# Kernel tuning notes

Hardware: AMD Instinct MI355X
Metric: run time of the kernel (lower is better)

## Reference

```python
import jax, jax.numpy as jnp
import numpy as np

B, H, S, D = 16, 12, 1024, 64  # batch, heads, seq, head_dim (dim=768, num_head=12)


def setup_inputs() -> dict:
    key = jax.random.key(0)
    ks = jax.random.split(key, 9)
    sc = 1.0 / np.sqrt(D)
    return {
        "x": jax.random.normal(ks[0], (B, H, S, D), dtype=jnp.float32),
        "Wq": jax.random.normal(ks[1], (D, D), dtype=jnp.float32) * sc,
        "bq": jax.random.normal(ks[2], (D,), dtype=jnp.float32) * 0.02,
        "Wk": jax.random.normal(ks[3], (D, D), dtype=jnp.float32) * sc,
        "bk": jax.random.normal(ks[4], (D,), dtype=jnp.float32) * 0.02,
        "Wv": jax.random.normal(ks[5], (D, D), dtype=jnp.float32) * sc,
        "bv": jax.random.normal(ks[6], (D,), dtype=jnp.float32) * 0.02,
        "Wo": jax.random.normal(ks[7], (D, D), dtype=jnp.float32) * sc,
        "bo": jax.random.normal(ks[8], (D,), dtype=jnp.float32) * 0.02,
    }


def reference(x, Wq, bq, Wk, bk, Wv, bv, Wo, bo):
    # torch Linear: y = x @ W^T + b, applied to last dim (head_dim)
    q = jnp.einsum("bhsd,ed->bhse", x, Wq) + bq
    k = jnp.einsum("bhsd,ed->bhse", x, Wk) + bk
    v = jnp.einsum("bhsd,ed->bhse", x, Wv) + bv
    scores = jnp.einsum("bhqd,bhkd->bhqk", q, k) / jnp.sqrt(jnp.float32(q.shape[-1]))
    attn = jax.nn.softmax(scores, axis=-1)
    out = jnp.einsum("bhqk,bhkd->bhqd", attn, v)
    out = jnp.einsum("bhsd,ed->bhse", out, Wo) + bo
    return out
```

## Files before the change

kernel.cpp:

```cpp
#include <hip/hip_runtime.h>
#include <math.h>


typedef __bf16 bf16x8 __attribute__((ext_vector_type(8)));
typedef float  f32x4  __attribute__((ext_vector_type(4)));

#define MFMA(a, b, c) __builtin_amdgcn_mfma_f32_16x16x32_bf16((a), (b), (c), 0, 0, 0)

static constexpr int S = 1024;
static constexpr int PAD = 72;
static constexpr size_t NE = 196608ull * 64ull;
static constexpr float QSCALE = 0.125f * 1.4426950408889634f;

__device__ inline unsigned long long pack4bf(float a, float b, float c, float d) {
    union { __bf16 h[4]; unsigned long long u; } pk;
    pk.h[0] = (__bf16)a; pk.h[1] = (__bf16)b; pk.h[2] = (__bf16)c; pk.h[3] = (__bf16)d;
    return pk.u;
}

union frag_u { bf16x8 v; unsigned long long u[2]; };

__global__ __launch_bounds__(256, 3) void projkv(
    const float* __restrict__ x,
    const float* __restrict__ Wk, const float* __restrict__ bk,
    const float* __restrict__ Wv, const float* __restrict__ bv,
    __bf16* __restrict__ gk, __bf16* __restrict__ gvt)
{
    __shared__ __align__(16) __bf16 lx[128][PAD];
    __shared__ __align__(16) __bf16 lbuf[128][PAD];
    __shared__ __align__(16) __bf16 lw[2][8][64][8];
    __shared__ float lb[2][64];

    const int tid = threadIdx.x;
    const int row_base = blockIdx.x * 128;

    #pragma unroll
    for (int i = tid * 4; i < 8192; i += 1024) {
        float4 v = *(const float4*)(x + (size_t)row_base * 64 + i);
        int r = i >> 6, c = i & 63;
        *(unsigned long long*)&lx[r][c] = pack4bf(v.x, v.y, v.z, v.w);
    }
    #pragma unroll
    for (int c = tid; c < 1024; c += 256) {
        int mtx = c >> 9, rest = c & 511;
        int fe = rest >> 6, ln = rest & 63;
        int mm = ln & 15, qq = ln >> 4;
        int et = fe >> 1, half = fe & 1;
        const float* src = (mtx ? Wv : Wk) + (size_t)(et * 16 + mm) * 64 + half * 32 + qq * 8;
        float4 u0 = *(const float4*)(src);
        float4 u1 = *(const float4*)(src + 4);
        *(unsigned long long*)&lw[mtx][fe][ln][0] = pack4bf(u0.x, u0.y, u0.z, u0.w);
        *(unsigned long long*)&lw[mtx][fe][ln][4] = pack4bf(u1.x, u1.y, u1.z, u1.w);
    }
    if (tid < 64) { lb[0][tid] = bk[tid]; lb[1][tid] = bv[tid]; }
    __syncthreads();

    const int w = tid >> 6, lane = tid & 63, m = lane & 15, quad = lane >> 4;
    const int bh = row_base >> 10;
    const int s_base = row_base & 1023;

    bf16x8 xf[2][2];
    #pragma unroll
    for (int g = 0; g < 2; g++) {
        xf[g][0] = *(const bf16x8*)&lx[w * 32 + g * 16 + m][quad * 8];
        xf[g][1] = *(const bf16x8*)&lx[w * 32 + g * 16 + m][32 + quad * 8];
    }

    #pragma unroll
    for (int et = 0; et < 4; et++) {
        bf16x8 wf0 = *(const bf16x8*)&lw[0][et * 2 + 0][lane][0];
        bf16x8 wf1 = *(const bf16x8*)&lw[0][et * 2 + 1][lane][0];
        float4 bias = *(const float4*)&lb[0][et * 16 + quad * 4];
        #pragma unroll
        for (int g = 0; g < 2; g++) {
            f32x4 acc = {0.f, 0.f, 0.f, 0.f};
            acc = MFMA(wf0, xf[g][0], acc);
            acc = MFMA(wf1, xf[g][1], acc);
            *(unsigned long long*)&lbuf[w * 32 + g * 16 + m][et * 16 + quad * 4] =
                pack4bf(acc[0] + bias.x, acc[1] + bias.y,
                        acc[2] + bias.z, acc[3] + bias.w);
        }
    }
    __syncthreads();
    #pragma unroll
    for (int it = 0; it < 4; it++) {
        int idx = it * 256 + tid;
        int row = idx >> 3, col = (idx & 7) * 8;
        *(uint4*)(gk + ((size_t)row_base + row) * 64 + col) = *(uint4*)&lbuf[row][col];
    }
    __syncthreads();

    __bf16 (*lvt)[136] = (__bf16(*)[136])&lbuf[0][0];
    #pragma unroll
    for (int et = 0; et < 4; et++) {
        bf16x8 wf0 = *(const bf16x8*)&lw[1][et * 2 + 0][lane][0];
        bf16x8 wf1 = *(const bf16x8*)&lw[1][et * 2 + 1][lane][0];
        const float bias = lb[1][et * 16 + m];
        #pragma unroll
        for (int g = 0; g < 2; g++) {
            f32x4 acc = {0.f, 0.f, 0.f, 0.f};
            acc = MFMA(xf[g][0], wf0, acc);
            acc = MFMA(xf[g][1], wf1, acc);
            const int tp = (2 * w + g) & 3;
            const int p0 = 64 * (w >> 1) + 32 * (tp >> 1) + 8 * quad + 4 * (tp & 1);
            *(unsigned long long*)&lvt[et * 16 + m][p0] =
                pack4bf(acc[0] + bias, acc[1] + bias, acc[2] + bias, acc[3] + bias);
        }
    }
    __syncthreads();
    #pragma unroll
    for (int it = 0; it < 4; it++) {
        int idx = it * 256 + tid;
        int row = idx >> 4, col = (idx & 15) * 8;
        *(uint4*)(gvt + ((size_t)bh * 64 + row) * 1024 + s_base + col) = *(uint4*)&lvt[row][col];
    }
}

__global__ __launch_bounds__(512, 4) void attn(
    const float* __restrict__ x,
    const float* __restrict__ Wq, const float* __restrict__ bq,
    const __bf16* __restrict__ gk, const __bf16* __restrict__ gvt,
    const float* __restrict__ Wo, const float* __restrict__ bo,
    float* __restrict__ out)
{
    __shared__ __align__(16) union {
        __bf16 xq[256][PAD];
        struct {
            __bf16 k[64][PAD];
            __bf16 v[64][PAD];
        } m;
    } L;

    const int tid = threadIdx.x;
    const int w = tid >> 6, lane = tid & 63, m = lane & 15, quad = lane >> 4;
    const int bh = blockIdx.x;
    const int q0 = blockIdx.y * 256 + w * 32;

    const float* xq32 = x + ((size_t)bh * 1024 + blockIdx.y * 256) * 64;
    #pragma unroll
    for (int i = tid * 4; i < 16384; i += 2048) {
        float4 v = *(const float4*)(xq32 + i);
        int r = i >> 6, c = i & 63;
        *(unsigned long long*)&L.xq[r][c] = pack4bf(v.x, v.y, v.z, v.w);
    }
    __syncthreads();

    bf16x8 xqf[2][2];
    #pragma unroll
    for (int g = 0; g < 2; g++) {
        xqf[g][0] = *(const bf16x8*)&L.xq[w * 32 + g * 16 + m][quad * 8];
        xqf[g][1] = *(const bf16x8*)&L.xq[w * 32 + g * 16 + m][32 + quad * 8];
    }
    #pragma unroll
    for (int et = 0; et < 4; et++) {
        const float* wqrow = Wq + (size_t)(et * 16 + m) * 64;
        float4 a0 = *(const float4*)(wqrow + quad * 8);
        float4 a1 = *(const float4*)(wqrow + quad * 8 + 4);
        float4 a2 = *(const float4*)(wqrow + 32 + quad * 8);
        float4 a3 = *(const float4*)(wqrow + 36 + quad * 8);
        frag_u wf0, wf1;
        wf0.u[0] = pack4bf(a0.x, a0.y, a0.z, a0.w);
        wf0.u[1] = pack4bf(a1.x, a1.y, a1.z, a1.w);
        wf1.u[0] = pack4bf(a2.x, a2.y, a2.z, a2.w);
        wf1.u[1] = pack4bf(a3.x, a3.y, a3.z, a3.w);
        float4 bias = *(const float4*)(bq + et * 16 + quad * 4);
        #pragma unroll
        for (int g = 0; g < 2; g++) {
            f32x4 acc = {0.f, 0.f, 0.f, 0.f};
            acc = MFMA(wf0.v, xqf[g][0], acc);
            acc = MFMA(wf1.v, xqf[g][1], acc);
            *(unsigned long long*)&L.xq[w * 32 + g * 16 + m][et * 16 + quad * 4] =
                pack4bf((acc[0] + bias.x) * QSCALE, (acc[1] + bias.y) * QSCALE,
                        (acc[2] + bias.z) * QSCALE, (acc[3] + bias.w) * QSCALE);
        }
    }
    bf16x8 qf[2][2];
    #pragma unroll
    for (int g = 0; g < 2; g++) {
        qf[g][0] = *(const bf16x8*)&L.xq[w * 32 + g * 16 + m][quad * 8];
        qf[g][1] = *(const bf16x8*)&L.xq[w * 32 + g * 16 + m][32 + quad * 8];
    }
    __syncthreads();

    f32x4 o[2][4];
    float lsum[2] = {0.f, 0.f};
    #pragma unroll
    for (int g = 0; g < 2; g++)
        #pragma unroll
        for (int n = 0; n < 4; n++) o[g][n] = {0.f, 0.f, 0.f, 0.f};

    const int sr = tid >> 3;
    const int sc = (tid & 7) * 8;
    const __bf16* kbase = gk + (size_t)bh * S * 64;
    const __bf16* vbase = gvt + (size_t)bh * 64 * 1024;

    for (int kb = 0; kb < 16; kb++) {
        __syncthreads();
        {
            const int nb = kb * 64;
            uint4 k0 = *(const uint4*)(kbase + (size_t)(nb + sr) * 64 + sc);
            uint4 v0 = *(const uint4*)(vbase + (size_t)sr * 1024 + nb + sc);
            *(uint4*)&L.m.k[sr][sc] = k0;
            *(uint4*)&L.m.v[sr][sc] = v0;
        }
        __syncthreads();

        __builtin_amdgcn_s_setprio(1);
        frag_u pb[2][2];
        #pragma unroll
        for (int t = 0; t < 4; t++) {
            bf16x8 ka0 = *(const bf16x8*)&L.m.k[t * 16 + m][quad * 8];
            bf16x8 ka1 = *(const bf16x8*)&L.m.k[t * 16 + m][32 + quad * 8];
            #pragma unroll
            for (int g = 0; g < 2; g++) {
                f32x4 acc = {0.f, 0.f, 0.f, 0.f};
                acc = MFMA(ka0, qf[g][0], acc);
                acc = MFMA(ka1, qf[g][1], acc);
                float e0 = __builtin_amdgcn_exp2f(acc[0]);
                float e1 = __builtin_amdgcn_exp2f(acc[1]);
                float e2 = __builtin_amdgcn_exp2f(acc[2]);
                float e3 = __builtin_amdgcn_exp2f(acc[3]);
                lsum[g] += (e0 + e1) + (e2 + e3);
                pb[g][t >> 1].u[t & 1] = pack4bf(e0, e1, e2, e3);
            }
        }
        #pragma unroll
        for (int n = 0; n < 4; n++) {
            bf16x8 va0 = *(const bf16x8*)&L.m.v[n * 16 + m][quad * 8];
            bf16x8 va1 = *(const bf16x8*)&L.m.v[n * 16 + m][32 + quad * 8];
            #pragma unroll
            for (int g = 0; g < 2; g++) {
                o[g][n] = MFMA(va0, pb[g][0].v, o[g][n]);
                o[g][n] = MFMA(va1, pb[g][1].v, o[g][n]);
            }
        }
        __builtin_amdgcn_s_setprio(0);
    }

    #pragma unroll
    for (int g = 0; g < 2; g++) {
        lsum[g] += __shfl_xor(lsum[g], 16);
        lsum[g] += __shfl_xor(lsum[g], 32);
    }

    bf16x8 wf[4][2];
    #pragma unroll
    for (int et = 0; et < 4; et++) {
        const float* worow = Wo + (size_t)(et * 16 + m) * 64;
        float4 c0 = *(const float4*)(worow + 4 * quad);
        float4 c1 = *(const float4*)(worow + 16 + 4 * quad);
        float4 c2 = *(const float4*)(worow + 32 + 4 * quad);
        float4 c3 = *(const float4*)(worow + 48 + 4 * quad);
        frag_u f0, f1;
        f0.u[0] = pack4bf(c0.x, c0.y, c0.z, c0.w);
        f0.u[1] = pack4bf(c1.x, c1.y, c1.z, c1.w);
        f1.u[0] = pack4bf(c2.x, c2.y, c2.z, c2.w);
        f1.u[1] = pack4bf(c3.x, c3.y, c3.z, c3.w);
        wf[et][0] = f0.v;
        wf[et][1] = f1.v;
    }
    float biasr[4];
    #pragma unroll
    for (int et = 0; et < 4; et++) biasr[et] = bo[et * 16 + m];

    #pragma unroll
    for (int g = 0; g < 2; g++) {
        const float inv = 1.f / lsum[g];
        frag_u af0, af1;
        af0.u[0] = pack4bf(o[g][0][0] * inv, o[g][0][1] * inv, o[g][0][2] * inv, o[g][0][3] * inv);
        af0.u[1] = pack4bf(o[g][1][0] * inv, o[g][1][1] * inv, o[g][1][2] * inv, o[g][1][3] * inv);
        af1.u[0] = pack4bf(o[g][2][0] * inv, o[g][2][1] * inv, o[g][2][2] * inv, o[g][2][3] * inv);
        af1.u[1] = pack4bf(o[g][3][0] * inv, o[g][3][1] * inv, o[g][3][2] * inv, o[g][3][3] * inv);
        #pragma unroll
        for (int et = 0; et < 4; et++) {
            f32x4 acc = {0.f, 0.f, 0.f, 0.f};
            acc = MFMA(af0.v, wf[et][0], acc);
            acc = MFMA(af1.v, wf[et][1], acc);
            #pragma unroll
            for (int r = 0; r < 4; r++) {
                size_t row = (size_t)bh * S + q0 + g * 16 + quad * 4 + r;
                out[row * 64 + et * 16 + m] = acc[r] + biasr[et];
            }
        }
    }
}

extern "C" void kernel_launch(void* const* d_in, const int* in_sizes, int n_in,
                              void* d_out, int out_size, void* d_ws, size_t ws_size,
                              hipStream_t stream) {
    const float* x  = (const float*)d_in[0];
    const float* Wq = (const float*)d_in[1];
    const float* bq = (const float*)d_in[2];
    const float* Wk = (const float*)d_in[3];
    const float* bk = (const float*)d_in[4];
    const float* Wv = (const float*)d_in[5];
    const float* bv = (const float*)d_in[6];
    const float* Wo = (const float*)d_in[7];
    const float* bo = (const float*)d_in[8];
    float* out = (float*)d_out;

    __bf16* gk  = (__bf16*)d_ws;
    __bf16* gvt = gk + NE;

    projkv<<<1536, 256, 0, stream>>>(x, Wk, bk, Wv, bv, gk, gvt);
    attn<<<dim3(192, 4), 512, 0, stream>>>(x, Wq, bq, gk, gvt, Wo, bo, out);
}
```

Measured before the change: 207.3 us.

## Load K/V fragments directly from global memory, dropping LDS staging and barriers

The attention loop no longer stages each 64-key K and V^T tile through shared memory with two block barriers per iteration. Each wave instead loads its MFMA operand fragments straight from global memory (relying on L1/L2 for reuse across the 8 waves) and splits the V loads into two halves interleaved with MFMAs. This removes LDS traffic and synchronisation but multiplies global/L2 load requests by the wave count and exposes per-wave load latency without a shared prefetch.

```diff
diff --git a/kernel.cpp b/kernel.cpp
--- a/kernel.cpp
+++ b/kernel.cpp
@@ -123,13 +123,7 @@
     const float* __restrict__ Wo, const float* __restrict__ bo,
     float* __restrict__ out)
 {
-    __shared__ __align__(16) union {
-        __bf16 xq[256][PAD];
-        struct {
-            __bf16 k[64][PAD];
-            __bf16 v[64][PAD];
-        } m;
-    } L;
+    __shared__ __align__(16) __bf16 xq[256][PAD];
 
     const int tid = threadIdx.x;
     const int w = tid >> 6, lane = tid & 63, m = lane & 15, quad = lane >> 4;
@@ -141,15 +135,15 @@
     for (int i = tid * 4; i < 16384; i += 2048) {
         float4 v = *(const float4*)(xq32 + i);
         int r = i >> 6, c = i & 63;
-        *(unsigned long long*)&L.xq[r][c] = pack4bf(v.x, v.y, v.z, v.w);
+        *(unsigned long long*)&xq[r][c] = pack4bf(v.x, v.y, v.z, v.w);
     }
     __syncthreads();
 
     bf16x8 xqf[2][2];
     #pragma unroll
     for (int g = 0; g < 2; g++) {
-        xqf[g][0] = *(const bf16x8*)&L.xq[w * 32 + g * 16 + m][quad * 8];
-        xqf[g][1] = *(const bf16x8*)&L.xq[w * 32 + g * 16 + m][32 + quad * 8];
+        xqf[g][0] = *(const bf16x8*)&xq[w * 32 + g * 16 + m][quad * 8];
+        xqf[g][1] = *(const bf16x8*)&xq[w * 32 + g * 16 + m][32 + quad * 8];
     }
     #pragma unroll
     for (int et = 0; et < 4; et++) {
@@ -169,7 +163,7 @@
             f32x4 acc = {0.f, 0.f, 0.f, 0.f};
             acc = MFMA(wf0.v, xqf[g][0], acc);
             acc = MFMA(wf1.v, xqf[g][1], acc);
-            *(unsigned long long*)&L.xq[w * 32 + g * 16 + m][et * 16 + quad * 4] =
+            *(unsigned long long*)&xq[w * 32 + g * 16 + m][et * 16 + quad * 4] =
                 pack4bf((acc[0] + bias.x) * QSCALE, (acc[1] + bias.y) * QSCALE,
                         (acc[2] + bias.z) * QSCALE, (acc[3] + bias.w) * QSCALE);
         }
@@ -177,10 +171,9 @@
     bf16x8 qf[2][2];
     #pragma unroll
     for (int g = 0; g < 2; g++) {
-        qf[g][0] = *(const bf16x8*)&L.xq[w * 32 + g * 16 + m][quad * 8];
-        qf[g][1] = *(const bf16x8*)&L.xq[w * 32 + g * 16 + m][32 + quad * 8];
-    }
-    __syncthreads();
+        qf[g][0] = *(const bf16x8*)&xq[w * 32 + g * 16 + m][quad * 8];
+        qf[g][1] = *(const bf16x8*)&xq[w * 32 + g * 16 + m][32 + quad * 8];
+    }
 
     f32x4 o[2][4];
     float lsum[2] = {0.f, 0.f};
@@ -189,33 +182,27 @@
         #pragma unroll
         for (int n = 0; n < 4; n++) o[g][n] = {0.f, 0.f, 0.f, 0.f};
 
-    const int sr = tid >> 3;
-    const int sc = (tid & 7) * 8;
     const __bf16* kbase = gk + (size_t)bh * S * 64;
     const __bf16* vbase = gvt + (size_t)bh * 64 * 1024;
 
     for (int kb = 0; kb < 16; kb++) {
-        __syncthreads();
-        {
-            const int nb = kb * 64;
-            uint4 k0 = *(const uint4*)(kbase + (size_t)(nb + sr) * 64 + sc);
-            uint4 v0 = *(const uint4*)(vbase + (size_t)sr * 1024 + nb + sc);
-            *(uint4*)&L.m.k[sr][sc] = k0;
-            *(uint4*)&L.m.v[sr][sc] = v0;
-        }
-        __syncthreads();
+        bf16x8 ka[4][2];
+        #pragma unroll
+        for (int t = 0; t < 4; t++) {
+            const __bf16* kr = kbase + (size_t)(kb * 64 + t * 16 + m) * 64;
+            ka[t][0] = *(const bf16x8*)(kr + quad * 8);
+            ka[t][1] = *(const bf16x8*)(kr + 32 + quad * 8);
+        }
 
         __builtin_amdgcn_s_setprio(1);
         frag_u pb[2][2];
         #pragma unroll
         for (int t = 0; t < 4; t++) {
-            bf16x8 ka0 = *(const bf16x8*)&L.m.k[t * 16 + m][quad * 8];
-            bf16x8 ka1 = *(const bf16x8*)&L.m.k[t * 16 + m][32 + quad * 8];
             #pragma unroll
             for (int g = 0; g < 2; g++) {
                 f32x4 acc = {0.f, 0.f, 0.f, 0.f};
-                acc = MFMA(ka0, qf[g][0], acc);
-                acc = MFMA(ka1, qf[g][1], acc);
+                acc = MFMA(ka[t][0], qf[g][0], acc);
+                acc = MFMA(ka[t][1], qf[g][1], acc);
                 float e0 = __builtin_amdgcn_exp2f(acc[0]);
                 float e1 = __builtin_amdgcn_exp2f(acc[1]);
                 float e2 = __builtin_amdgcn_exp2f(acc[2]);
@@ -224,17 +211,30 @@
                 pb[g][t >> 1].u[t & 1] = pack4bf(e0, e1, e2, e3);
             }
         }
-        #pragma unroll
-        for (int n = 0; n < 4; n++) {
-            bf16x8 va0 = *(const bf16x8*)&L.m.v[n * 16 + m][quad * 8];
-            bf16x8 va1 = *(const bf16x8*)&L.m.v[n * 16 + m][32 + quad * 8];
+        __builtin_amdgcn_s_setprio(0);
+
+        #pragma unroll
+        for (int nh = 0; nh < 2; nh++) {
+            bf16x8 va[2][2];
             #pragma unroll
-            for (int g = 0; g < 2; g++) {
-                o[g][n] = MFMA(va0, pb[g][0].v, o[g][n]);
-                o[g][n] = MFMA(va1, pb[g][1].v, o[g][n]);
+            for (int n2 = 0; n2 < 2; n2++) {
+                const int n = nh * 2 + n2;
+                const __bf16* vr = vbase + (size_t)(n * 16 + m) * 1024 + kb * 64;
+                va[n2][0] = *(const bf16x8*)(vr + quad * 8);
+                va[n2][1] = *(const bf16x8*)(vr + 32 + quad * 8);
             }
-        }
-        __builtin_amdgcn_s_setprio(0);
+            __builtin_amdgcn_s_setprio(1);
+            #pragma unroll
+            for (int n2 = 0; n2 < 2; n2++) {
+                const int n = nh * 2 + n2;
+                #pragma unroll
+                for (int g = 0; g < 2; g++) {
+                    o[g][n] = MFMA(va[n2][0], pb[g][0].v, o[g][n]);
+                    o[g][n] = MFMA(va[n2][1], pb[g][1].v, o[g][n]);
+                }
+            }
+            __builtin_amdgcn_s_setprio(0);
+        }
     }
 
     #pragma unroll
```

After: 317.0 us. 1.53x slower.
